# Optimization experiments

Measured on AMD Instinct MI355X. Metric: run time of the kernel, lower is better.

Reference implementation:

```python
import jax, jax.numpy as jnp
import numpy as np

N = 50000          # total residues (nodes)
E = 800000         # contact edges, avg degree 16
F_IN = 1280        # ESM embedding dim
H = 256            # hidden
L = 4              # num_layers
B = 100            # proteins in batch
MAX_NODES = 500    # residues per protein (uniform -> static to_dense_batch shape)


def setup_inputs() -> dict:
    key = jax.random.key(0)
    ks = jax.random.split(key, 16)
    s = 0.02
    inp = {
        "seq": jax.random.randint(ks[0], (N,), 0, 26),
        "edge_index": jax.random.randint(ks[1], (2, E), 0, N),
        "esm_token": jax.random.normal(ks[2], (N, F_IN), jnp.float32),
        "batch": jnp.arange(N) // MAX_NODES,
        # lin0
        "lin0_W": jax.random.normal(ks[3], (F_IN, H), jnp.float32) * s,
        "lin0_b": jnp.zeros((H,), jnp.float32),
        # WeightConv1 per layer: lin1 (root), lin2 (neighbor), lin3 (mask head)
        "wc_W1": jax.random.normal(ks[4], (L, H, H), jnp.float32) * s,
        "wc_b1": jnp.zeros((L, H), jnp.float32),
        "wc_W2": jax.random.normal(ks[5], (L, H, H), jnp.float32) * s,
        "wc_b2": jnp.zeros((L, H), jnp.float32),
        "wc_W3": jax.random.normal(ks[6], (L, H, H), jnp.float32) * s,
        "wc_b3": jnp.zeros((L, H), jnp.float32),
        # SparseConv per layer: neighbor weight + bias, root weight
        "sc_Wn": jax.random.normal(ks[7], (L, H, H), jnp.float32) * s,
        "sc_bn": jnp.zeros((L, H), jnp.float32),
        "sc_Wr": jax.random.normal(ks[8], (L, H, H), jnp.float32) * s,
    }
    return inp


def reference(seq, edge_index, esm_token, batch,
              lin0_W, lin0_b,
              wc_W1, wc_b1, wc_W2, wc_b2, wc_W3, wc_b3,
              sc_Wn, sc_bn, sc_Wr):
    src, dst = edge_index[0], edge_index[1]
    x = esm_token @ lin0_W + lin0_b              # [N, H]
    mask_val = None
    xs = []
    for i in range(L):
        # ---- WeightConv1: learned edge-conditioned node mask ----
        xm = x if mask_val is None else x * mask_val
        h_nb = xm @ wc_W2[i] + wc_b2[i]          # neighbor transform [N, H]
        agg = jax.ops.segment_sum(h_nb[src], dst, num_segments=N)
        h = jax.nn.relu(agg + xm @ wc_W1[i] + wc_b1[i])
        mask_val = jax.nn.sigmoid(h @ wc_W3[i] + wc_b3[i])   # [N, H]
        # ---- SparseConv: mask-gated sparse aggregation ----
        xg = x * mask_val
        agg2 = jax.ops.segment_sum(xg[src], dst, num_segments=N)
        x = jax.nn.relu(agg2 @ sc_Wn[i] + sc_bn[i] + x @ sc_Wr[i])
        xs.append(x)
    feat = jnp.concatenate(xs, axis=-1)          # jumping-knowledge cat [N, L*H]
    # ---- to_dense_batch ----
    counts = jax.ops.segment_sum(jnp.ones((N,), jnp.int32), batch, num_segments=B)
    starts = jnp.cumsum(counts) - counts
    pos = jnp.arange(N) - starts[batch]
    dense = jnp.zeros((B, MAX_NODES, L * H), feat.dtype).at[batch, pos].set(feat)
    node_mask = jnp.zeros((B, MAX_NODES), bool).at[batch, pos].set(True)
    return dense, node_mask
```

## Files before the change

kernel.cpp:

```cpp
#include <hip/hip_runtime.h>

#define NNODES 50000
#define HDIM 256
#define NLAYERS 4
#define NEDGES 800000
#define FIN 1280
#define LDOUT 1024

typedef _Float16 f16;
typedef __attribute__((ext_vector_type(8))) _Float16 f16x8;
typedef __attribute__((ext_vector_type(4))) _Float16 f16x4;
typedef __attribute__((ext_vector_type(4))) float f32x4;

enum { SRC_H = 0, SRC_MULH = 1, SRC_ADDRELU_HH = 2, SRC_CATH = 3 };
enum { EPI_W2W1H = 0, EPI_MASKXG = 1, EPI_CATH = 2 };

template<int SRC, int EPI, int KTILES>
__global__ __launch_bounds__(256) void mgemm_k(
    const f16*  __restrict__ A3,
    const f16*  __restrict__ A5,
    const f16*  __restrict__ A4,
    const f16*  __restrict__ Xh,
    const f16*  __restrict__ Wt,
    const f16*  __restrict__ Wt2,
    const float* __restrict__ bias,
    const float* __restrict__ bias2,
    float* __restrict__ Cf, int ldc,
    f16*  __restrict__ Ch,
    f16*  __restrict__ Ch2)
{
    constexpr int K = KTILES * 64;
    __shared__ f16 Asm[2][4096];

    const int row0 = blockIdx.x * 64;
    const int by = blockIdx.y;
    const int tid = threadIdx.x;
    const int wv = tid >> 6;
    const int l = tid & 63;

    f32x4 acc[4][4] = {};

    const int sr = tid >> 2;
    const int sc0 = (tid & 3) * 16;
    const int grow = row0 + sr;
    const bool rok = grow < NNODES;
    const int lane_base0 =
        (((sc0 >> 5) * 4 + (sr >> 4)) * 64 + (sr & 15) + (((sc0 & 31) >> 3) * 16)) * 8;
    const int lane_base1 = lane_base0 + 128;

    const f16* Wsel = (EPI == EPI_W2W1H && by) ? Wt2 : Wt;
    const f16* bp[4];
    #pragma unroll
    for (int cf = 0; cf < 4; ++cf)
        bp[cf] = Wsel + (size_t)(wv * 64 + cf * 16 + (l & 15)) * K + ((l >> 4) * 8);

    struct SReg { f16x8 h0, h1, g0, g1; };
    SReg RA, RB;

    auto LOAD = [&](SReg& r, int kt) {
        if (!rok) return;
        const int k0 = kt * 64 + sc0;
        if constexpr (SRC == SRC_CATH) {
            const f16* p = (k0 < HDIM)
                ? (A3 + (size_t)grow * HDIM + k0)
                : (A4 + (size_t)grow * HDIM + (k0 - HDIM));
            r.h0 = *(const f16x8*)p;  r.h1 = *(const f16x8*)(p + 8);
        } else {
            const f16* p = A3 + (size_t)grow * HDIM + k0;
            r.h0 = *(const f16x8*)p;  r.h1 = *(const f16x8*)(p + 8);
            if constexpr (SRC == SRC_MULH || SRC == SRC_ADDRELU_HH) {
                const f16* q = A5 + (size_t)grow * HDIM + k0;
                r.g0 = *(const f16x8*)q;  r.g1 = *(const f16x8*)(q + 8);
            }
        }
    };

    auto COMMIT = [&](const SReg& r, int b) {
        f16x8 av0, av1;
        #pragma unroll
        for (int i = 0; i < 8; ++i) { av0[i] = (f16)0.f; av1[i] = (f16)0.f; }
        if (rok) {
            if constexpr (SRC == SRC_H || SRC == SRC_CATH) {
                av0 = r.h0; av1 = r.h1;
            } else if constexpr (SRC == SRC_MULH) {
                #pragma unroll
                for (int i = 0; i < 8; ++i) {
                    av0[i] = (f16)((float)r.h0[i] * (float)r.g0[i]);
                    av1[i] = (f16)((float)r.h1[i] * (float)r.g1[i]);
                }
            } else {
                #pragma unroll
                for (int i = 0; i < 8; ++i) {
                    av0[i] = (f16)fmaxf((float)r.h0[i] + (float)r.g0[i], 0.f);
                    av1[i] = (f16)fmaxf((float)r.h1[i] + (float)r.g1[i], 0.f);
                }
            }
        }
        *(f16x8*)(&Asm[b][lane_base0]) = av0;
        *(f16x8*)(&Asm[b][lane_base1]) = av1;
    };

    auto TILE = [&](int b, int kt) {
        f16x8 af[4][2];
        #pragma unroll
        for (int rf = 0; rf < 4; ++rf)
            #pragma unroll
            for (int kb = 0; kb < 2; ++kb)
                af[rf][kb] = *(const f16x8*)(&Asm[b][((kb * 4 + rf) * 64 + l) * 8]);
        f16x8 bfr[4][2];
        #pragma unroll
        for (int cf = 0; cf < 4; ++cf) {
            bfr[cf][0] = *(const f16x8*)(bp[cf] + kt * 64);
            bfr[cf][1] = *(const f16x8*)(bp[cf] + kt * 64 + 32);
        }
        #pragma unroll
        for (int cf = 0; cf < 4; ++cf)
            #pragma unroll
            for (int rf = 0; rf < 4; ++rf)
                #pragma unroll
                for (int kb = 0; kb < 2; ++kb)
                    acc[rf][cf] = __builtin_amdgcn_mfma_f32_16x16x32_f16(
                        af[rf][kb], bfr[cf][kb], acc[rf][cf], 0, 0, 0);
    };

    LOAD(RA, 0);
    COMMIT(RA, 0);
    if (KTILES > 1) LOAD(RB, 1);
    #pragma unroll
    for (int kt2 = 0; kt2 < KTILES; kt2 += 2) {
        __syncthreads();
        TILE(0, kt2);
        if (kt2 + 1 < KTILES) COMMIT(RB, 1);
        if (kt2 + 2 < KTILES) LOAD(RA, kt2 + 2);
        if (kt2 + 1 < KTILES) {
            __syncthreads();
            TILE(1, kt2 + 1);
            if (kt2 + 2 < KTILES) COMMIT(RA, 0);
            if (kt2 + 3 < KTILES) LOAD(RB, kt2 + 3);
        }
    }

    #pragma unroll
    for (int rf = 0; rf < 4; ++rf) {
        #pragma unroll
        for (int j = 0; j < 4; ++j) {
            const int row = row0 + rf * 16 + ((l >> 4) * 4) + j;
            if (row >= NNODES) continue;
            #pragma unroll
            for (int cf = 0; cf < 4; ++cf) {
                const int col = wv * 64 + cf * 16 + (l & 15);
                float v = acc[rf][cf][j];
                if constexpr (EPI == EPI_W2W1H) {
                    if (by == 0) Ch[(size_t)row * HDIM + col]  = (f16)(v + bias[col]);
                    else         Ch2[(size_t)row * HDIM + col] = (f16)(v + bias2[col]);
                } else if constexpr (EPI == EPI_MASKXG) {
                    const float m = 1.f / (1.f + expf(-(v + bias[col])));
                    Ch2[(size_t)row * HDIM + col] = (f16)m;
                    Ch[(size_t)row * HDIM + col] =
                        (f16)((float)Xh[(size_t)row * HDIM + col] * m);
                } else {
                    const float r = fmaxf(v + bias[col], 0.f);
                    Cf[(size_t)row * ldc + col] = r;
                    Ch[(size_t)row * HDIM + col] = (f16)r;
                }
            }
        }
    }
}

template<int KTILES>
__global__ __launch_bounds__(256) void lin0_k(
    const float* __restrict__ A1, int lda1,
    const f16*  __restrict__ WtA, const f16* __restrict__ WtB,
    float* __restrict__ Cf, float* __restrict__ Cf2)
{
    constexpr int K = KTILES * 64;
    __shared__ f16 Asm[2][4096];

    const int row0 = blockIdx.x * 64;
    const int by = blockIdx.y;
    const int tid = threadIdx.x;
    const int wv = tid >> 6;
    const int l = tid & 63;

    f32x4 acc[4][4] = {};

    const int sr = tid >> 2;
    const int sc0 = (tid & 3) * 16;
    const int grow = row0 + sr;
    const bool rok = grow < NNODES;
    const int kg = by * K;
    const int lane_base0 =
        (((sc0 >> 5) * 4 + (sr >> 4)) * 64 + (sr & 15) + (((sc0 & 31) >> 3) * 16)) * 8;
    const int lane_base1 = lane_base0 + 128;

    const f16* Wsel = by ? WtB : WtA;
    const f16* bp[4];
    #pragma unroll
    for (int cf = 0; cf < 4; ++cf)
        bp[cf] = Wsel + (size_t)(wv * 64 + cf * 16 + (l & 15)) * K + ((l >> 4) * 8);

    struct SReg { float4 f0, f1, f2, f3; };
    SReg RA, RB;

    auto LOAD = [&](SReg& r, int kt) {
        if (!rok) return;
        const float* p = A1 + (size_t)grow * lda1 + kg + kt * 64 + sc0;
        r.f0 = *(const float4*)(p + 0);  r.f1 = *(const float4*)(p + 4);
        r.f2 = *(const float4*)(p + 8);  r.f3 = *(const float4*)(p + 12);
    };

    auto COMMIT = [&](const SReg& r, int b) {
        f16x8 av0, av1;
        #pragma unroll
        for (int i = 0; i < 8; ++i) { av0[i] = (f16)0.f; av1[i] = (f16)0.f; }
        if (rok) {
            av0[0]=(f16)r.f0.x; av0[1]=(f16)r.f0.y; av0[2]=(f16)r.f0.z; av0[3]=(f16)r.f0.w;
            av0[4]=(f16)r.f1.x; av0[5]=(f16)r.f1.y; av0[6]=(f16)r.f1.z; av0[7]=(f16)r.f1.w;
            av1[0]=(f16)r.f2.x; av1[1]=(f16)r.f2.y; av1[2]=(f16)r.f2.z; av1[3]=(f16)r.f2.w;
            av1[4]=(f16)r.f3.x; av1[5]=(f16)r.f3.y; av1[6]=(f16)r.f3.z; av1[7]=(f16)r.f3.w;
        }
        *(f16x8*)(&Asm[b][lane_base0]) = av0;
        *(f16x8*)(&Asm[b][lane_base1]) = av1;
    };

    auto TILE = [&](int b, int kt) {
        f16x8 af[4][2];
        #pragma unroll
        for (int rf = 0; rf < 4; ++rf)
            #pragma unroll
            for (int kb = 0; kb < 2; ++kb)
                af[rf][kb] = *(const f16x8*)(&Asm[b][((kb * 4 + rf) * 64 + l) * 8]);
        f16x8 bfr[4][2];
        #pragma unroll
        for (int cf = 0; cf < 4; ++cf) {
            bfr[cf][0] = *(const f16x8*)(bp[cf] + kt * 64);
            bfr[cf][1] = *(const f16x8*)(bp[cf] + kt * 64 + 32);
        }
        #pragma unroll
        for (int cf = 0; cf < 4; ++cf)
            #pragma unroll
            for (int rf = 0; rf < 4; ++rf)
                #pragma unroll
                for (int kb = 0; kb < 2; ++kb)
                    acc[rf][cf] = __builtin_amdgcn_mfma_f32_16x16x32_f16(
                        af[rf][kb], bfr[cf][kb], acc[rf][cf], 0, 0, 0);
    };

    LOAD(RA, 0);
    COMMIT(RA, 0);
    if (KTILES > 1) LOAD(RB, 1);
    #pragma unroll
    for (int kt2 = 0; kt2 < KTILES; kt2 += 2) {
        __syncthreads();
        TILE(0, kt2);
        if (kt2 + 1 < KTILES) COMMIT(RB, 1);
        if (kt2 + 2 < KTILES) LOAD(RA, kt2 + 2);
        if (kt2 + 1 < KTILES) {
            __syncthreads();
            TILE(1, kt2 + 1);
            if (kt2 + 2 < KTILES) COMMIT(RA, 0);
            if (kt2 + 3 < KTILES) LOAD(RB, kt2 + 3);
        }
    }

    #pragma unroll
    for (int rf = 0; rf < 4; ++rf) {
        #pragma unroll
        for (int j = 0; j < 4; ++j) {
            const int row = row0 + rf * 16 + ((l >> 4) * 4) + j;
            if (row >= NNODES) continue;
            #pragma unroll
            for (int cf = 0; cf < 4; ++cf) {
                const int col = wv * 64 + cf * 16 + (l & 15);
                (by ? Cf2 : Cf)[(size_t)row * HDIM + col] = acc[rf][cf][j];
            }
        }
    }
}

__global__ __launch_bounds__(256) void combine_k(
    const float* __restrict__ P0, const float* __restrict__ P1,
    const float* __restrict__ b, f16* __restrict__ xh)
{
    const int t = blockIdx.x * 256 + threadIdx.x;
    const int row = t >> 6;
    const int c = (t & 63) * 4;
    if (row >= NNODES) return;
    const float4 a = *(const float4*)(P0 + (size_t)row * HDIM + c);
    const float4 d = *(const float4*)(P1 + (size_t)row * HDIM + c);
    const float4 bb = *(const float4*)(b + c);
    f16x4 r;
    r[0] = (f16)(a.x + d.x + bb.x); r[1] = (f16)(a.y + d.y + bb.y);
    r[2] = (f16)(a.z + d.z + bb.z); r[3] = (f16)(a.w + d.w + bb.w);
    *(f16x4*)(xh + (size_t)row * HDIM + c) = r;
}

__global__ __launch_bounds__(256) void pack_all_k(
    const float* __restrict__ lin0_W,
    const float* __restrict__ W2, const float* __restrict__ W1,
    const float* __restrict__ W3,
    const float* __restrict__ Wn, const float* __restrict__ Wr,
    f16* __restrict__ dst)
{
    int idx = blockIdx.x * 256 + threadIdx.x;
    const int total = 163840 * 2 + 262144 * 3 + 524288;
    if (idx >= total) return;
    f16* d = dst + idx;
    if (idx < 327680) {
        const int half = idx / 163840;
        int r = idx % 163840;
        const int col = r / 640, k = r % 640;
        *d = (f16)lin0_W[(size_t)(k + half * 640) * 256 + col];
        return;
    }
    idx -= 327680;
    if (idx < 786432) {
        const int which = idx / 262144;
        int r = idx % 262144;
        const int i = r / 65536; r %= 65536;
        const int col = r / 256, k = r % 256;
        const float* W = (which == 0) ? W2 : (which == 1) ? W1 : W3;
        *d = (f16)W[(size_t)i * 65536 + k * 256 + col];
        return;
    }
    idx -= 786432;
    const int i = idx / 131072; int r = idx % 131072;
    const int col = r / 512, k = r % 512;
    *d = (f16)(k < 256 ? Wn[(size_t)i * 65536 + k * 256 + col]
                       : Wr[(size_t)i * 65536 + (k - 256) * 256 + col]);
}

__global__ __launch_bounds__(256) void count_k(
    const int* __restrict__ dstIdx, int* __restrict__ counts)
{
    const int e = blockIdx.x * 256 + threadIdx.x;
    if (e < NEDGES) atomicAdd(&counts[dstIdx[e]], 1);
}

__global__ __launch_bounds__(1024) void scan_k(
    const int* __restrict__ counts, int* __restrict__ starts)
{
    __shared__ int sm[1024];
    __shared__ int s_off;
    if (threadIdx.x == 0) s_off = 0;
    __syncthreads();
    for (int base = 0; base < NNODES; base += 1024) {
        const int i = base + threadIdx.x;
        const int v = (i < NNODES) ? counts[i] : 0;
        sm[threadIdx.x] = v;
        __syncthreads();
        for (int ofs = 1; ofs < 1024; ofs <<= 1) {
            const int t = (threadIdx.x >= ofs) ? sm[threadIdx.x - ofs] : 0;
            __syncthreads();
            sm[threadIdx.x] += t;
            __syncthreads();
        }
        const int incl = sm[threadIdx.x];
        const int off = s_off;
        if (i < NNODES) starts[i] = off + incl - v;
        __syncthreads();
        if (threadIdx.x == 1023) s_off = off + incl;
        __syncthreads();
    }
    if (threadIdx.x == 0) starts[NNODES] = s_off;
}

__global__ __launch_bounds__(256) void fillcsr_k(
    const int* __restrict__ srcIdx, const int* __restrict__ dstIdx,
    int* __restrict__ cursor, int* __restrict__ csr)
{
    const int e = blockIdx.x * 256 + threadIdx.x;
    if (e >= NEDGES) return;
    const int d = dstIdx[e];
    const int p = atomicAdd(&cursor[d], 1);
    csr[p] = srcIdx[e];
}

__global__ __launch_bounds__(256) void gather_g_k(
    const f16* __restrict__ rows, const int* __restrict__ csr,
    const int* __restrict__ starts, f16* __restrict__ outp)
{
    const int node = (blockIdx.x * 256 + threadIdx.x) >> 6;
    const int lane = threadIdx.x & 63;
    if (node >= NNODES) return;
    const int e0 = starts[node], e1 = starts[node + 1];
    float a0=0,a1=0,a2=0,a3=0, b0=0,b1=0,b2=0,b3=0;
    int e = e0;
    for (; e + 3 < e1; e += 4) {
        const int s0=csr[e], s1=csr[e+1], s2=csr[e+2], s3=csr[e+3];
        f16x4 v0 = *(const f16x4*)(rows + (size_t)s0 * HDIM + lane * 4);
        f16x4 v1 = *(const f16x4*)(rows + (size_t)s1 * HDIM + lane * 4);
        f16x4 v2 = *(const f16x4*)(rows + (size_t)s2 * HDIM + lane * 4);
        f16x4 v3 = *(const f16x4*)(rows + (size_t)s3 * HDIM + lane * 4);
        a0 += (float)v0[0] + (float)v2[0]; a1 += (float)v0[1] + (float)v2[1];
        a2 += (float)v0[2] + (float)v2[2]; a3 += (float)v0[3] + (float)v2[3];
        b0 += (float)v1[0] + (float)v3[0]; b1 += (float)v1[1] + (float)v3[1];
        b2 += (float)v1[2] + (float)v3[2]; b3 += (float)v1[3] + (float)v3[3];
    }
    for (; e < e1; ++e) {
        const int s0 = csr[e];
        f16x4 v0 = *(const f16x4*)(rows + (size_t)s0 * HDIM + lane * 4);
        a0 += (float)v0[0]; a1 += (float)v0[1]; a2 += (float)v0[2]; a3 += (float)v0[3];
    }
    f16x4 r;
    r[0] = (f16)(a0 + b0); r[1] = (f16)(a1 + b1);
    r[2] = (f16)(a2 + b2); r[3] = (f16)(a3 + b3);
    *(f16x4*)(outp + (size_t)node * HDIM + lane * 4) = r;
}

__global__ __launch_bounds__(256) void fill1_k(float* __restrict__ p, int n)
{
    const int t = blockIdx.x * 256 + threadIdx.x;
    if (t < n) p[t] = 1.0f;
}

extern "C" void kernel_launch(void* const* d_in, const int* in_sizes, int n_in,
                              void* d_out, int out_size, void* d_ws, size_t ws_size,
                              hipStream_t stream)
{
    const int*   edge   = (const int*)d_in[1];
    const int*   src    = edge;
    const int*   dst    = edge + NEDGES;
    const float* esm    = (const float*)d_in[2];
    const float* lin0_W = (const float*)d_in[4];
    const float* lin0_b = (const float*)d_in[5];
    const float* wc_W1  = (const float*)d_in[6];
    const float* wc_b1  = (const float*)d_in[7];
    const float* wc_W2  = (const float*)d_in[8];
    const float* wc_b2  = (const float*)d_in[9];
    const float* wc_W3  = (const float*)d_in[10];
    const float* wc_b3  = (const float*)d_in[11];
    const float* sc_Wn  = (const float*)d_in[12];
    const float* sc_bn  = (const float*)d_in[13];
    const float* sc_Wr  = (const float*)d_in[14];
    float* out = (float*)d_out;

    const size_t NH = (size_t)NNODES * HDIM;
    float* ws    = (float*)d_ws;
    float* part0 = ws;
    float* part1 = ws + NH;
    f16*   xh    = (f16*)(ws + 2 * NH);
    f16*   hnb   = xh + NH;
    f16*   agg1  = hnb + NH;
    f16*   agg2  = agg1 + NH;
    f16*   xw1h  = agg2 + NH;
    f16*   maskh = xw1h + NH;
    f16*   wpack = maskh + NH;
    f16*   lin0tA = wpack;
    f16*   lin0tB = lin0tA + 163840;
    f16*   W2t   = lin0tB + 163840;
    f16*   W1t   = W2t + 262144;
    f16*   W3t   = W1t + 262144;
    f16*   WtC   = W3t + 262144;
    int*   iws    = (int*)(WtC + 524288);
    int*   counts = iws;
    int*   starts = iws + NNODES;
    int*   cursor = iws + 2 * NNODES + 1;
    int*   csr    = iws + 3 * NNODES + 2;

    const dim3 blk(256);
    const int gemmGrid = (NNODES + 63) / 64;
    const int edgeGrid = (NEDGES + 255) / 256;
    const int waveGrid = (NNODES * 64) / 256;

    hipMemsetAsync(counts, 0, NNODES * sizeof(int), stream);
    count_k<<<edgeGrid, blk, 0, stream>>>(dst, counts);
    scan_k<<<1, 1024, 0, stream>>>(counts, starts);
    hipMemcpyAsync(cursor, starts, NNODES * sizeof(int),
                   hipMemcpyDeviceToDevice, stream);
    fillcsr_k<<<edgeGrid, blk, 0, stream>>>(src, dst, cursor, csr);

    pack_all_k<<<(1638400 + 255) / 256, blk, 0, stream>>>(
        lin0_W, wc_W2, wc_W1, wc_W3, sc_Wn, sc_Wr, wpack);

    lin0_k<10><<<dim3(gemmGrid, 2), blk, 0, stream>>>(
        esm, FIN, lin0tA, lin0tB, part0, part1);
    combine_k<<<waveGrid, blk, 0, stream>>>(part0, part1, lin0_b, xh);

    for (int i = 0; i < NLAYERS; ++i) {
        const size_t bo = (size_t)i * HDIM;
        const f16* w2 = W2t + i * 65536;
        const f16* w1 = W1t + i * 65536;
        const f16* w3 = W3t + i * 65536;
        const f16* wc = WtC + i * 131072;

        if (i == 0) {
            mgemm_k<SRC_H, EPI_W2W1H, 4><<<dim3(gemmGrid, 2), blk, 0, stream>>>(
                xh, nullptr, nullptr, nullptr, w2, w1,
                wc_b2 + bo, wc_b1 + bo, nullptr, 0, hnb, xw1h);
        } else {
            mgemm_k<SRC_MULH, EPI_W2W1H, 4><<<dim3(gemmGrid, 2), blk, 0, stream>>>(
                xh, maskh, nullptr, nullptr, w2, w1,
                wc_b2 + bo, wc_b1 + bo, nullptr, 0, hnb, xw1h);
        }
        gather_g_k<<<waveGrid, blk, 0, stream>>>(hnb, csr, starts, agg1);
        mgemm_k<SRC_ADDRELU_HH, EPI_MASKXG, 4><<<gemmGrid, blk, 0, stream>>>(
            agg1, xw1h, nullptr, xh, w3, nullptr,
            wc_b3 + bo, nullptr, nullptr, 0, hnb, maskh);
        gather_g_k<<<waveGrid, blk, 0, stream>>>(hnb, csr, starts, agg2);
        mgemm_k<SRC_CATH, EPI_CATH, 8><<<gemmGrid, blk, 0, stream>>>(
            agg2, nullptr, xh, nullptr, wc, nullptr,
            sc_bn + bo, nullptr, out + (size_t)i * HDIM, LDOUT, xh, nullptr);
    }

    const size_t maskOff = (size_t)NNODES * LDOUT;
    fill1_k<<<(NNODES + 255) / 256, blk, 0, stream>>>(out + maskOff, NNODES);
}
```

Measured before the change: 1.378 ms.

## Fuse CSR neighbor gathers into the following GEMMs via shared-memory A tiles

```diff
diff --git a/kernel.cpp b/kernel.cpp
--- a/kernel.cpp
+++ b/kernel.cpp
@@ -12,24 +12,22 @@
 typedef __attribute__((ext_vector_type(4))) _Float16 f16x4;
 typedef __attribute__((ext_vector_type(4))) float f32x4;
 
-enum { SRC_H = 0, SRC_MULH = 1, SRC_ADDRELU_HH = 2, SRC_CATH = 3 };
-enum { EPI_W2W1H = 0, EPI_MASKXG = 1, EPI_CATH = 2 };
-
-template<int SRC, int EPI, int KTILES>
-__global__ __launch_bounds__(256) void mgemm_k(
+enum { SRC_H = 0, SRC_MULH = 1 };
+
+
+template<int SRC>
+__global__ __launch_bounds__(256) void w2w1_k(
     const f16*  __restrict__ A3,
     const f16*  __restrict__ A5,
-    const f16*  __restrict__ A4,
-    const f16*  __restrict__ Xh,
     const f16*  __restrict__ Wt,
     const f16*  __restrict__ Wt2,
     const float* __restrict__ bias,
     const float* __restrict__ bias2,
-    float* __restrict__ Cf, int ldc,
     f16*  __restrict__ Ch,
     f16*  __restrict__ Ch2)
 {
-    constexpr int K = KTILES * 64;
+    constexpr int KTILES = 4;
+    constexpr int K = 256;
     __shared__ f16 Asm[2][4096];
 
     const int row0 = blockIdx.x * 64;
@@ -48,7 +46,7 @@
         (((sc0 >> 5) * 4 + (sr >> 4)) * 64 + (sr & 15) + (((sc0 & 31) >> 3) * 16)) * 8;
     const int lane_base1 = lane_base0 + 128;
 
-    const f16* Wsel = (EPI == EPI_W2W1H && by) ? Wt2 : Wt;
+    const f16* Wsel = by ? Wt2 : Wt;
     const f16* bp[4];
     #pragma unroll
     for (int cf = 0; cf < 4; ++cf)
@@ -60,18 +58,11 @@
     auto LOAD = [&](SReg& r, int kt) {
         if (!rok) return;
         const int k0 = kt * 64 + sc0;
-        if constexpr (SRC == SRC_CATH) {
-            const f16* p = (k0 < HDIM)
-                ? (A3 + (size_t)grow * HDIM + k0)
-                : (A4 + (size_t)grow * HDIM + (k0 - HDIM));
-            r.h0 = *(const f16x8*)p;  r.h1 = *(const f16x8*)(p + 8);
-        } else {
-            const f16* p = A3 + (size_t)grow * HDIM + k0;
-            r.h0 = *(const f16x8*)p;  r.h1 = *(const f16x8*)(p + 8);
-            if constexpr (SRC == SRC_MULH || SRC == SRC_ADDRELU_HH) {
-                const f16* q = A5 + (size_t)grow * HDIM + k0;
-                r.g0 = *(const f16x8*)q;  r.g1 = *(const f16x8*)(q + 8);
-            }
+        const f16* p = A3 + (size_t)grow * HDIM + k0;
+        r.h0 = *(const f16x8*)p;  r.h1 = *(const f16x8*)(p + 8);
+        if constexpr (SRC == SRC_MULH) {
+            const f16* q = A5 + (size_t)grow * HDIM + k0;
+            r.g0 = *(const f16x8*)q;  r.g1 = *(const f16x8*)(q + 8);
         }
     };
 
@@ -80,19 +71,13 @@
         #pragma unroll
         for (int i = 0; i < 8; ++i) { av0[i] = (f16)0.f; av1[i] = (f16)0.f; }
         if (rok) {
-            if constexpr (SRC == SRC_H || SRC == SRC_CATH) {
+            if constexpr (SRC == SRC_H) {
                 av0 = r.h0; av1 = r.h1;
-            } else if constexpr (SRC == SRC_MULH) {
+            } else {
                 #pragma unroll
                 for (int i = 0; i < 8; ++i) {
                     av0[i] = (f16)((float)r.h0[i] * (float)r.g0[i]);
                     av1[i] = (f16)((float)r.h1[i] * (float)r.g1[i]);
-                }
-            } else {
-                #pragma unroll
-                for (int i = 0; i < 8; ++i) {
-                    av0[i] = (f16)fmaxf((float)r.h0[i] + (float)r.g0[i], 0.f);
-                    av1[i] = (f16)fmaxf((float)r.h1[i] + (float)r.g1[i], 0.f);
                 }
             }
         }
@@ -125,19 +110,17 @@
 
     LOAD(RA, 0);
     COMMIT(RA, 0);
-    if (KTILES > 1) LOAD(RB, 1);
+    LOAD(RB, 1);
     #pragma unroll
     for (int kt2 = 0; kt2 < KTILES; kt2 += 2) {
         __syncthreads();
         TILE(0, kt2);
-        if (kt2 + 1 < KTILES) COMMIT(RB, 1);
+        COMMIT(RB, 1);
         if (kt2 + 2 < KTILES) LOAD(RA, kt2 + 2);
-        if (kt2 + 1 < KTILES) {
-            __syncthreads();
-            TILE(1, kt2 + 1);
-            if (kt2 + 2 < KTILES) COMMIT(RA, 0);
-            if (kt2 + 3 < KTILES) LOAD(RB, kt2 + 3);
-        }
+        __syncthreads();
+        TILE(1, kt2 + 1);
+        if (kt2 + 2 < KTILES) COMMIT(RA, 0);
+        if (kt2 + 3 < KTILES) LOAD(RB, kt2 + 3);
     }
 
     #pragma unroll
@@ -150,19 +133,265 @@
             for (int cf = 0; cf < 4; ++cf) {
                 const int col = wv * 64 + cf * 16 + (l & 15);
                 float v = acc[rf][cf][j];
-                if constexpr (EPI == EPI_W2W1H) {
-                    if (by == 0) Ch[(size_t)row * HDIM + col]  = (f16)(v + bias[col]);
-                    else         Ch2[(size_t)row * HDIM + col] = (f16)(v + bias2[col]);
-                } else if constexpr (EPI == EPI_MASKXG) {
-                    const float m = 1.f / (1.f + expf(-(v + bias[col])));
-                    Ch2[(size_t)row * HDIM + col] = (f16)m;
-                    Ch[(size_t)row * HDIM + col] =
-                        (f16)((float)Xh[(size_t)row * HDIM + col] * m);
-                } else {
-                    const float r = fmaxf(v + bias[col], 0.f);
-                    Cf[(size_t)row * ldc + col] = r;
-                    Ch[(size_t)row * HDIM + col] = (f16)r;
+                if (by == 0) Ch[(size_t)row * HDIM + col]  = (f16)(v + bias[col]);
+                else         Ch2[(size_t)row * HDIM + col] = (f16)(v + bias2[col]);
+            }
+        }
+    }
+}
+
+__global__ __launch_bounds__(256) void g1m_k(
+    const f16* __restrict__ hnb,
+    const int* __restrict__ csr, const int* __restrict__ starts,
+    const f16* __restrict__ xw1h,
+    const f16* __restrict__ xcur,
+    const f16* __restrict__ W3t,
+    const float* __restrict__ b3,
+    f16* __restrict__ maskh,
+    f16* __restrict__ xg)
+{
+    __shared__ f16 Afr[32 * 64 * 8];
+
+    const int tid = threadIdx.x;
+    const int l = tid & 63;
+    const int wv = tid >> 6;
+    const int row0 = blockIdx.x * 64;
+
+    const int c = l * 4;
+    const int region_c = ((c >> 6) << 3) + (((c >> 5) & 1) << 2);
+    const int slot_c = (((c & 31) >> 3) << 4);
+    for (int t = 0; t < 16; ++t) {
+        const int srow = wv * 16 + t;
+        const int node = row0 + srow;
+        float r0 = 0.f, r1 = 0.f, r2 = 0.f, r3 = 0.f;
+        if (node < NNODES) {
+            const int e0 = starts[node], e1 = starts[node + 1];
+            float s0=0,s1=0,s2=0,s3=0, u0=0,u1=0,u2=0,u3=0;
+            int e = e0;
+            for (; e + 3 < e1; e += 4) {
+                const int q0=csr[e], q1=csr[e+1], q2=csr[e+2], q3=csr[e+3];
+                f16x4 v0 = *(const f16x4*)(hnb + (size_t)q0 * HDIM + c);
+                f16x4 v1 = *(const f16x4*)(hnb + (size_t)q1 * HDIM + c);
+                f16x4 v2 = *(const f16x4*)(hnb + (size_t)q2 * HDIM + c);
+                f16x4 v3 = *(const f16x4*)(hnb + (size_t)q3 * HDIM + c);
+                s0 += (float)v0[0] + (float)v2[0]; s1 += (float)v0[1] + (float)v2[1];
+                s2 += (float)v0[2] + (float)v2[2]; s3 += (float)v0[3] + (float)v2[3];
+                u0 += (float)v1[0] + (float)v3[0]; u1 += (float)v1[1] + (float)v3[1];
+                u2 += (float)v1[2] + (float)v3[2]; u3 += (float)v1[3] + (float)v3[3];
+            }
+            for (; e < e1; ++e) {
+                const int q0 = csr[e];
+                f16x4 v0 = *(const f16x4*)(hnb + (size_t)q0 * HDIM + c);
+                s0 += (float)v0[0]; s1 += (float)v0[1];
+                s2 += (float)v0[2]; s3 += (float)v0[3];
+            }
+            const f16x4 w = *(const f16x4*)(xw1h + (size_t)node * HDIM + c);
+            r0 = fmaxf(s0 + u0 + (float)w[0], 0.f);
+            r1 = fmaxf(s1 + u1 + (float)w[1], 0.f);
+            r2 = fmaxf(s2 + u2 + (float)w[2], 0.f);
+            r3 = fmaxf(s3 + u3 + (float)w[3], 0.f);
+        }
+        f16x4 st;
+        st[0] = (f16)r0; st[1] = (f16)r1; st[2] = (f16)r2; st[3] = (f16)r3;
+        const int region = region_c + (srow >> 4);
+        const int slot = slot_c + (srow & 15);
+        *(f16x4*)(&Afr[((region << 6) + slot) * 8 + (c & 7)]) = st;
+    }
+    __syncthreads();
+
+    const f16* bp[4];
+    #pragma unroll
+    for (int cf = 0; cf < 4; ++cf)
+        bp[cf] = W3t + (size_t)(wv * 64 + cf * 16 + (l & 15)) * 256 + ((l >> 4) * 8);
+
+    f32x4 acc[4][4] = {};
+    f16x8 bC[4][2], bN[4][2];
+    #pragma unroll
+    for (int cf = 0; cf < 4; ++cf) {
+        bC[cf][0] = *(const f16x8*)(bp[cf]);
+        bC[cf][1] = *(const f16x8*)(bp[cf] + 32);
+    }
+    #pragma unroll
+    for (int kt = 0; kt < 4; ++kt) {
+        if (kt < 3) {
+            #pragma unroll
+            for (int cf = 0; cf < 4; ++cf) {
+                bN[cf][0] = *(const f16x8*)(bp[cf] + (kt + 1) * 64);
+                bN[cf][1] = *(const f16x8*)(bp[cf] + (kt + 1) * 64 + 32);
+            }
+        }
+        f16x8 af[4][2];
+        #pragma unroll
+        for (int rf = 0; rf < 4; ++rf)
+            #pragma unroll
+            for (int kb = 0; kb < 2; ++kb)
+                af[rf][kb] = *(const f16x8*)(&Afr[((kt * 8 + kb * 4 + rf) * 64 + l) * 8]);
+        #pragma unroll
+        for (int cf = 0; cf < 4; ++cf)
+            #pragma unroll
+            for (int rf = 0; rf < 4; ++rf)
+                #pragma unroll
+                for (int kb = 0; kb < 2; ++kb)
+                    acc[rf][cf] = __builtin_amdgcn_mfma_f32_16x16x32_f16(
+                        af[rf][kb], bC[cf][kb], acc[rf][cf], 0, 0, 0);
+        if (kt < 3) {
+            #pragma unroll
+            for (int cf = 0; cf < 4; ++cf) {
+                bC[cf][0] = bN[cf][0];  bC[cf][1] = bN[cf][1];
+            }
+        }
+    }
+
+    #pragma unroll
+    for (int rf = 0; rf < 4; ++rf) {
+        #pragma unroll
+        for (int j = 0; j < 4; ++j) {
+            const int row = row0 + rf * 16 + ((l >> 4) * 4) + j;
+            if (row >= NNODES) continue;
+            #pragma unroll
+            for (int cf = 0; cf < 4; ++cf) {
+                const int col = wv * 64 + cf * 16 + (l & 15);
+                const float m = 1.f / (1.f + expf(-(acc[rf][cf][j] + b3[col])));
+                maskh[(size_t)row * HDIM + col] = (f16)m;
+                xg[(size_t)row * HDIM + col] =
+                    (f16)((float)xcur[(size_t)row * HDIM + col] * m);
+            }
+        }
+    }
+}
+
+__global__ __launch_bounds__(256) void g2c_k(
+    const f16* __restrict__ xg,
+    const int* __restrict__ csr, const int* __restrict__ starts,
+    const f16* __restrict__ xcur,
+    const f16* __restrict__ WtC,
+    const float* __restrict__ bn,
+    float* __restrict__ outp,
+    f16* __restrict__ xnew)
+{
+    __shared__ f16 Afr[32 * 64 * 8];
+
+    const int tid = threadIdx.x;
+    const int l = tid & 63;
+    const int wv = tid >> 6;
+    const int row0 = blockIdx.x * 64;
+
+    const int c = l * 4;
+    const int region_c = ((c >> 6) << 3) + (((c >> 5) & 1) << 2);
+    const int slot_c = (((c & 31) >> 3) << 4);
+    for (int t = 0; t < 16; ++t) {
+        const int srow = wv * 16 + t;
+        const int node = row0 + srow;
+        float r0 = 0.f, r1 = 0.f, r2 = 0.f, r3 = 0.f;
+        if (node < NNODES) {
+            const int e0 = starts[node], e1 = starts[node + 1];
+            float s0=0,s1=0,s2=0,s3=0, u0=0,u1=0,u2=0,u3=0;
+            int e = e0;
+            for (; e + 3 < e1; e += 4) {
+                const int q0=csr[e], q1=csr[e+1], q2=csr[e+2], q3=csr[e+3];
+                f16x4 v0 = *(const f16x4*)(xg + (size_t)q0 * HDIM + c);
+                f16x4 v1 = *(const f16x4*)(xg + (size_t)q1 * HDIM + c);
+                f16x4 v2 = *(const f16x4*)(xg + (size_t)q2 * HDIM + c);
+                f16x4 v3 = *(const f16x4*)(xg + (size_t)q3 * HDIM + c);
+                s0 += (float)v0[0] + (float)v2[0]; s1 += (float)v0[1] + (float)v2[1];
+                s2 += (float)v0[2] + (float)v2[2]; s3 += (float)v0[3] + (float)v2[3];
+                u0 += (float)v1[0] + (float)v3[0]; u1 += (float)v1[1] + (float)v3[1];
+                u2 += (float)v1[2] + (float)v3[2]; u3 += (float)v1[3] + (float)v3[3];
+            }
+            for (; e < e1; ++e) {
+                const int q0 = csr[e];
+                f16x4 v0 = *(const f16x4*)(xg + (size_t)q0 * HDIM + c);
+                s0 += (float)v0[0]; s1 += (float)v0[1];
+                s2 += (float)v0[2]; s3 += (float)v0[3];
+            }
+            r0 = s0 + u0; r1 = s1 + u1; r2 = s2 + u2; r3 = s3 + u3;
+        }
+        f16x4 st;
+        st[0] = (f16)r0; st[1] = (f16)r1; st[2] = (f16)r2; st[3] = (f16)r3;
+        const int region = region_c + (srow >> 4);
+        const int slot = slot_c + (srow & 15);
+        *(f16x4*)(&Afr[((region << 6) + slot) * 8 + (c & 7)]) = st;
+    }
+    __syncthreads();
+
+    const f16* bp[4];
+    #pragma unroll
+    for (int cf = 0; cf < 4; ++cf)
+        bp[cf] = WtC + (size_t)(wv * 64 + cf * 16 + (l & 15)) * 512 + ((l >> 4) * 8);
+
+    bool rvalid[4];
+    const f16* xrow[4];
+    #pragma unroll
+    for (int rf = 0; rf < 4; ++rf) {
+        const int ar = row0 + rf * 16 + (l & 15);
+        rvalid[rf] = ar < NNODES;
+        xrow[rf] = xcur + (size_t)ar * HDIM + ((l >> 4) * 8);
+    }
+
+    f32x4 acc[4][4] = {};
+    f16x8 bC[4][2], bN[4][2];
+    #pragma unroll
+    for (int cf = 0; cf < 4; ++cf) {
+        bC[cf][0] = *(const f16x8*)(bp[cf]);
+        bC[cf][1] = *(const f16x8*)(bp[cf] + 32);
+    }
+    #pragma unroll
+    for (int kt = 0; kt < 8; ++kt) {
+        if (kt < 7) {
+            #pragma unroll
+            for (int cf = 0; cf < 4; ++cf) {
+                bN[cf][0] = *(const f16x8*)(bp[cf] + (kt + 1) * 64);
+                bN[cf][1] = *(const f16x8*)(bp[cf] + (kt + 1) * 64 + 32);
+            }
+        }
+        f16x8 af[4][2];
+        if (kt < 4) {
+            #pragma unroll
+            for (int rf = 0; rf < 4; ++rf)
+                #pragma unroll
+                for (int kb = 0; kb < 2; ++kb)
+                    af[rf][kb] = *(const f16x8*)(&Afr[((kt * 8 + kb * 4 + rf) * 64 + l) * 8]);
+        } else {
+            #pragma unroll
+            for (int rf = 0; rf < 4; ++rf)
+                #pragma unroll
+                for (int kb = 0; kb < 2; ++kb) {
+                    f16x8 v;
+                    #pragma unroll
+                    for (int i = 0; i < 8; ++i) v[i] = (f16)0.f;
+                    if (rvalid[rf])
+                        v = *(const f16x8*)(xrow[rf] + (kt - 4) * 64 + kb * 32);
+                    af[rf][kb] = v;
                 }
+        }
+        #pragma unroll
+        for (int cf = 0; cf < 4; ++cf)
+            #pragma unroll
+            for (int rf = 0; rf < 4; ++rf)
+                #pragma unroll
+                for (int kb = 0; kb < 2; ++kb)
+                    acc[rf][cf] = __builtin_amdgcn_mfma_f32_16x16x32_f16(
+                        af[rf][kb], bC[cf][kb], acc[rf][cf], 0, 0, 0);
+        if (kt < 7) {
+            #pragma unroll
+            for (int cf = 0; cf < 4; ++cf) {
+                bC[cf][0] = bN[cf][0];  bC[cf][1] = bN[cf][1];
+            }
+        }
+    }
+
+    #pragma unroll
+    for (int rf = 0; rf < 4; ++rf) {
+        #pragma unroll
+        for (int j = 0; j < 4; ++j) {
+            const int row = row0 + rf * 16 + ((l >> 4) * 4) + j;
+            if (row >= NNODES) continue;
+            #pragma unroll
+            for (int cf = 0; cf < 4; ++cf) {
+                const int col = wv * 64 + cf * 16 + (l & 15);
+                const float r = fmaxf(acc[rf][cf][j] + bn[col], 0.f);
+                outp[(size_t)row * LDOUT + col] = r;
+                xnew[(size_t)row * HDIM + col] = (f16)r;
             }
         }
     }
@@ -375,38 +604,6 @@
     const int d = dstIdx[e];
     const int p = atomicAdd(&cursor[d], 1);
     csr[p] = srcIdx[e];
-}
-
-__global__ __launch_bounds__(256) void gather_g_k(
-    const f16* __restrict__ rows, const int* __restrict__ csr,
-    const int* __restrict__ starts, f16* __restrict__ outp)
-{
-    const int node = (blockIdx.x * 256 + threadIdx.x) >> 6;
-    const int lane = threadIdx.x & 63;
-    if (node >= NNODES) return;
-    const int e0 = starts[node], e1 = starts[node + 1];
-    float a0=0,a1=0,a2=0,a3=0, b0=0,b1=0,b2=0,b3=0;
-    int e = e0;
-    for (; e + 3 < e1; e += 4) {
-        const int s0=csr[e], s1=csr[e+1], s2=csr[e+2], s3=csr[e+3];
-        f16x4 v0 = *(const f16x4*)(rows + (size_t)s0 * HDIM + lane * 4);
-        f16x4 v1 = *(const f16x4*)(rows + (size_t)s1 * HDIM + lane * 4);
-        f16x4 v2 = *(const f16x4*)(rows + (size_t)s2 * HDIM + lane * 4);
-        f16x4 v3 = *(const f16x4*)(rows + (size_t)s3 * HDIM + lane * 4);
-        a0 += (float)v0[0] + (float)v2[0]; a1 += (float)v0[1] + (float)v2[1];
-        a2 += (float)v0[2] + (float)v2[2]; a3 += (float)v0[3] + (float)v2[3];
-        b0 += (float)v1[0] + (float)v3[0]; b1 += (float)v1[1] + (float)v3[1];
-        b2 += (float)v1[2] + (float)v3[2]; b3 += (float)v1[3] + (float)v3[3];
-    }
-    for (; e < e1; ++e) {
-        const int s0 = csr[e];
-        f16x4 v0 = *(const f16x4*)(rows + (size_t)s0 * HDIM + lane * 4);
-        a0 += (float)v0[0]; a1 += (float)v0[1]; a2 += (float)v0[2]; a3 += (float)v0[3];
-    }
-    f16x4 r;
-    r[0] = (f16)(a0 + b0); r[1] = (f16)(a1 + b1);
-    r[2] = (f16)(a2 + b2); r[3] = (f16)(a3 + b3);
-    *(f16x4*)(outp + (size_t)node * HDIM + lane * 4) = r;
 }
 
 __global__ __launch_bounds__(256) void fill1_k(float* __restrict__ p, int n)
@@ -440,13 +637,13 @@
     float* ws    = (float*)d_ws;
     float* part0 = ws;
     float* part1 = ws + NH;
-    f16*   xh    = (f16*)(ws + 2 * NH);
-    f16*   hnb   = xh + NH;
-    f16*   agg1  = hnb + NH;
-    f16*   agg2  = agg1 + NH;
-    f16*   xw1h  = agg2 + NH;
+    f16*   xhA   = (f16*)(ws + 2 * NH);
+    f16*   xhB   = xhA + NH;
+    f16*   hnb   = xhB + NH;
+    f16*   xw1h  = hnb + NH;
     f16*   maskh = xw1h + NH;
-    f16*   wpack = maskh + NH;
+    f16*   xg    = maskh + NH;
+    f16*   wpack = xg + NH;
     f16*   lin0tA = wpack;
     f16*   lin0tB = lin0tA + 163840;
     f16*   W2t   = lin0tB + 163840;
@@ -476,7 +673,7 @@
 
     lin0_k<10><<<dim3(gemmGrid, 2), blk, 0, stream>>>(
         esm, FIN, lin0tA, lin0tB, part0, part1);
-    combine_k<<<waveGrid, blk, 0, stream>>>(part0, part1, lin0_b, xh);
+    combine_k<<<waveGrid, blk, 0, stream>>>(part0, part1, lin0_b, xhA);
 
     for (int i = 0; i < NLAYERS; ++i) {
         const size_t bo = (size_t)i * HDIM;
@@ -484,24 +681,21 @@
         const f16* w1 = W1t + i * 65536;
         const f16* w3 = W3t + i * 65536;
         const f16* wc = WtC + i * 131072;
+        const f16* xcur = (i & 1) ? xhB : xhA;
+        f16*       xnew = (i & 1) ? xhA : xhB;
 
         if (i == 0) {
-            mgemm_k<SRC_H, EPI_W2W1H, 4><<<dim3(gemmGrid, 2), blk, 0, stream>>>(
-                xh, nullptr, nullptr, nullptr, w2, w1,
-                wc_b2 + bo, wc_b1 + bo, nullptr, 0, hnb, xw1h);
+            w2w1_k<SRC_H><<<dim3(gemmGrid, 2), blk, 0, stream>>>(
+                xcur, nullptr, w2, w1, wc_b2 + bo, wc_b1 + bo, hnb, xw1h);
         } else {
-            mgemm_k<SRC_MULH, EPI_W2W1H, 4><<<dim3(gemmGrid, 2), blk, 0, stream>>>(
-                xh, maskh, nullptr, nullptr, w2, w1,
-                wc_b2 + bo, wc_b1 + bo, nullptr, 0, hnb, xw1h);
-        }
-        gather_g_k<<<waveGrid, blk, 0, stream>>>(hnb, csr, starts, agg1);
-        mgemm_k<SRC_ADDRELU_HH, EPI_MASKXG, 4><<<gemmGrid, blk, 0, stream>>>(
-            agg1, xw1h, nullptr, xh, w3, nullptr,
-            wc_b3 + bo, nullptr, nullptr, 0, hnb, maskh);
-        gather_g_k<<<waveGrid, blk, 0, stream>>>(hnb, csr, starts, agg2);
-        mgemm_k<SRC_CATH, EPI_CATH, 8><<<gemmGrid, blk, 0, stream>>>(
-            agg2, nullptr, xh, nullptr, wc, nullptr,
-            sc_bn + bo, nullptr, out + (size_t)i * HDIM, LDOUT, xh, nullptr);
+            w2w1_k<SRC_MULH><<<dim3(gemmGrid, 2), blk, 0, stream>>>(
+                xcur, maskh, w2, w1, wc_b2 + bo, wc_b1 + bo, hnb, xw1h);
+        }
+        g1m_k<<<gemmGrid, blk, 0, stream>>>(
+            hnb, csr, starts, xw1h, xcur, w3, wc_b3 + bo, maskh, xg);
+        g2c_k<<<gemmGrid, blk, 0, stream>>>(
+            xg, csr, starts, xcur, wc, sc_bn + bo,
+            out + (size_t)i * HDIM, xnew);
     }
 
     const size_t maskOff = (size_t)NNODES * LDOUT;
```

Result: slower. 1.934 ms (+40.3%).

## Aggregate before transform in WeightConv and fuse W2/W1 into one concat GEMM

Applied to the files above, without the earlier changes.

```diff
diff --git a/kernel.cpp b/kernel.cpp
--- a/kernel.cpp
+++ b/kernel.cpp
@@ -12,28 +12,27 @@
 typedef __attribute__((ext_vector_type(4))) _Float16 f16x4;
 typedef __attribute__((ext_vector_type(4))) float f32x4;
 
-enum { SRC_H = 0, SRC_MULH = 1, SRC_ADDRELU_HH = 2, SRC_CATH = 3 };
-enum { EPI_W2W1H = 0, EPI_MASKXG = 1, EPI_CATH = 2 };
+enum { SRC_H = 0, SRC_CATH = 1 };
+enum { EPI_HRELU = 0, EPI_MASKXG = 1, EPI_CATH2 = 2 };
 
 template<int SRC, int EPI, int KTILES>
 __global__ __launch_bounds__(256) void mgemm_k(
     const f16*  __restrict__ A3,
-    const f16*  __restrict__ A5,
     const f16*  __restrict__ A4,
     const f16*  __restrict__ Xh,
+    const int*  __restrict__ deg,
     const f16*  __restrict__ Wt,
-    const f16*  __restrict__ Wt2,
     const float* __restrict__ bias,
     const float* __restrict__ bias2,
     float* __restrict__ Cf, int ldc,
     f16*  __restrict__ Ch,
-    f16*  __restrict__ Ch2)
+    f16*  __restrict__ Ch2,
+    f16*  __restrict__ Ch3)
 {
     constexpr int K = KTILES * 64;
     __shared__ f16 Asm[2][4096];
 
     const int row0 = blockIdx.x * 64;
-    const int by = blockIdx.y;
     const int tid = threadIdx.x;
     const int wv = tid >> 6;
     const int l = tid & 63;
@@ -48,54 +47,32 @@
         (((sc0 >> 5) * 4 + (sr >> 4)) * 64 + (sr & 15) + (((sc0 & 31) >> 3) * 16)) * 8;
     const int lane_base1 = lane_base0 + 128;
 
-    const f16* Wsel = (EPI == EPI_W2W1H && by) ? Wt2 : Wt;
     const f16* bp[4];
     #pragma unroll
     for (int cf = 0; cf < 4; ++cf)
-        bp[cf] = Wsel + (size_t)(wv * 64 + cf * 16 + (l & 15)) * K + ((l >> 4) * 8);
-
-    struct SReg { f16x8 h0, h1, g0, g1; };
+        bp[cf] = Wt + (size_t)(wv * 64 + cf * 16 + (l & 15)) * K + ((l >> 4) * 8);
+
+    struct SReg { f16x8 h0, h1; };
     SReg RA, RB;
 
     auto LOAD = [&](SReg& r, int kt) {
         if (!rok) return;
         const int k0 = kt * 64 + sc0;
+        const f16* p;
         if constexpr (SRC == SRC_CATH) {
-            const f16* p = (k0 < HDIM)
-                ? (A3 + (size_t)grow * HDIM + k0)
-                : (A4 + (size_t)grow * HDIM + (k0 - HDIM));
-            r.h0 = *(const f16x8*)p;  r.h1 = *(const f16x8*)(p + 8);
+            p = (k0 < HDIM) ? (A3 + (size_t)grow * HDIM + k0)
+                            : (A4 + (size_t)grow * HDIM + (k0 - HDIM));
         } else {
-            const f16* p = A3 + (size_t)grow * HDIM + k0;
-            r.h0 = *(const f16x8*)p;  r.h1 = *(const f16x8*)(p + 8);
-            if constexpr (SRC == SRC_MULH || SRC == SRC_ADDRELU_HH) {
-                const f16* q = A5 + (size_t)grow * HDIM + k0;
-                r.g0 = *(const f16x8*)q;  r.g1 = *(const f16x8*)(q + 8);
-            }
-        }
+            p = A3 + (size_t)grow * HDIM + k0;
+        }
+        r.h0 = *(const f16x8*)p;  r.h1 = *(const f16x8*)(p + 8);
     };
 
     auto COMMIT = [&](const SReg& r, int b) {
         f16x8 av0, av1;
         #pragma unroll
         for (int i = 0; i < 8; ++i) { av0[i] = (f16)0.f; av1[i] = (f16)0.f; }
-        if (rok) {
-            if constexpr (SRC == SRC_H || SRC == SRC_CATH) {
-                av0 = r.h0; av1 = r.h1;
-            } else if constexpr (SRC == SRC_MULH) {
-                #pragma unroll
-                for (int i = 0; i < 8; ++i) {
-                    av0[i] = (f16)((float)r.h0[i] * (float)r.g0[i]);
-                    av1[i] = (f16)((float)r.h1[i] * (float)r.g1[i]);
-                }
-            } else {
-                #pragma unroll
-                for (int i = 0; i < 8; ++i) {
-                    av0[i] = (f16)fmaxf((float)r.h0[i] + (float)r.g0[i], 0.f);
-                    av1[i] = (f16)fmaxf((float)r.h1[i] + (float)r.g1[i], 0.f);
-                }
-            }
-        }
+        if (rok) { av0 = r.h0; av1 = r.h1; }
         *(f16x8*)(&Asm[b][lane_base0]) = av0;
         *(f16x8*)(&Asm[b][lane_base1]) = av1;
     };
@@ -150,9 +127,10 @@
             for (int cf = 0; cf < 4; ++cf) {
                 const int col = wv * 64 + cf * 16 + (l & 15);
                 float v = acc[rf][cf][j];
-                if constexpr (EPI == EPI_W2W1H) {
-                    if (by == 0) Ch[(size_t)row * HDIM + col]  = (f16)(v + bias[col]);
-                    else         Ch2[(size_t)row * HDIM + col] = (f16)(v + bias2[col]);
+                if constexpr (EPI == EPI_HRELU) {
+                    const float dv = (float)deg[row];
+                    v = fmaxf(v + dv * bias[col] + bias2[col], 0.f);
+                    Ch[(size_t)row * HDIM + col] = (f16)v;
                 } else if constexpr (EPI == EPI_MASKXG) {
                     const float m = 1.f / (1.f + expf(-(v + bias[col])));
                     Ch2[(size_t)row * HDIM + col] = (f16)m;
@@ -162,6 +140,8 @@
                     const float r = fmaxf(v + bias[col], 0.f);
                     Cf[(size_t)row * ldc + col] = r;
                     Ch[(size_t)row * HDIM + col] = (f16)r;
+                    Ch3[(size_t)row * HDIM + col] =
+                        (f16)(r * (float)Xh[(size_t)row * HDIM + col]);
                 }
             }
         }
@@ -171,8 +151,8 @@
 template<int KTILES>
 __global__ __launch_bounds__(256) void lin0_k(
     const float* __restrict__ A1, int lda1,
-    const f16*  __restrict__ WtA, const f16* __restrict__ WtB,
-    float* __restrict__ Cf, float* __restrict__ Cf2)
+    const f16*  __restrict__ WtBase,
+    f16* __restrict__ parts)
 {
     constexpr int K = KTILES * 64;
     __shared__ f16 Asm[2][4096];
@@ -194,7 +174,7 @@
         (((sc0 >> 5) * 4 + (sr >> 4)) * 64 + (sr & 15) + (((sc0 & 31) >> 3) * 16)) * 8;
     const int lane_base1 = lane_base0 + 128;
 
-    const f16* Wsel = by ? WtB : WtA;
+    const f16* Wsel = WtBase + (size_t)by * 256 * K;
     const f16* bp[4];
     #pragma unroll
     for (int cf = 0; cf < 4; ++cf)
@@ -264,6 +244,7 @@
         }
     }
 
+    f16* Ph = parts + (size_t)by * NNODES * HDIM;
     #pragma unroll
     for (int rf = 0; rf < 4; ++rf) {
         #pragma unroll
@@ -273,27 +254,33 @@
             #pragma unroll
             for (int cf = 0; cf < 4; ++cf) {
                 const int col = wv * 64 + cf * 16 + (l & 15);
-                (by ? Cf2 : Cf)[(size_t)row * HDIM + col] = acc[rf][cf][j];
+                Ph[(size_t)row * HDIM + col] = (f16)acc[rf][cf][j];
             }
         }
     }
 }
 
-__global__ __launch_bounds__(256) void combine_k(
-    const float* __restrict__ P0, const float* __restrict__ P1,
-    const float* __restrict__ b, f16* __restrict__ xh)
+__global__ __launch_bounds__(256) void combine4_k(
+    const f16* __restrict__ parts, const float* __restrict__ b,
+    f16* __restrict__ xh)
 {
     const int t = blockIdx.x * 256 + threadIdx.x;
     const int row = t >> 6;
     const int c = (t & 63) * 4;
     if (row >= NNODES) return;
-    const float4 a = *(const float4*)(P0 + (size_t)row * HDIM + c);
-    const float4 d = *(const float4*)(P1 + (size_t)row * HDIM + c);
+    const size_t NH = (size_t)NNODES * HDIM;
+    const size_t off = (size_t)row * HDIM + c;
+    f16x4 p0 = *(const f16x4*)(parts + off);
+    f16x4 p1 = *(const f16x4*)(parts + NH + off);
+    f16x4 p2 = *(const f16x4*)(parts + 2 * NH + off);
+    f16x4 p3 = *(const f16x4*)(parts + 3 * NH + off);
     const float4 bb = *(const float4*)(b + c);
     f16x4 r;
-    r[0] = (f16)(a.x + d.x + bb.x); r[1] = (f16)(a.y + d.y + bb.y);
-    r[2] = (f16)(a.z + d.z + bb.z); r[3] = (f16)(a.w + d.w + bb.w);
-    *(f16x4*)(xh + (size_t)row * HDIM + c) = r;
+    r[0] = (f16)((float)p0[0] + (float)p1[0] + (float)p2[0] + (float)p3[0] + bb.x);
+    r[1] = (f16)((float)p0[1] + (float)p1[1] + (float)p2[1] + (float)p3[1] + bb.y);
+    r[2] = (f16)((float)p0[2] + (float)p1[2] + (float)p2[2] + (float)p3[2] + bb.z);
+    r[3] = (f16)((float)p0[3] + (float)p1[3] + (float)p2[3] + (float)p3[3] + bb.w);
+    *(f16x4*)(xh + off) = r;
 }
 
 __global__ __launch_bounds__(256) void pack_all_k(
@@ -304,27 +291,34 @@
     f16* __restrict__ dst)
 {
     int idx = blockIdx.x * 256 + threadIdx.x;
-    const int total = 163840 * 2 + 262144 * 3 + 524288;
+    const int total = 327680 + 524288 + 262144 + 524288;
     if (idx >= total) return;
     f16* d = dst + idx;
     if (idx < 327680) {
-        const int half = idx / 163840;
-        int r = idx % 163840;
-        const int col = r / 640, k = r % 640;
-        *d = (f16)lin0_W[(size_t)(k + half * 640) * 256 + col];
+        const int q = idx / 81920;
+        int r = idx % 81920;
+        const int col = r / 320, k = r % 320;
+        *d = (f16)lin0_W[(size_t)(k + q * 320) * 256 + col];
         return;
     }
     idx -= 327680;
-    if (idx < 786432) {
-        const int which = idx / 262144;
-        int r = idx % 262144;
-        const int i = r / 65536; r %= 65536;
+    if (idx < 524288) {
+        const int i = idx / 131072;
+        int r = idx % 131072;
+        const int col = r / 512, k = r % 512;
+        *d = (f16)(k < 256 ? W2[(size_t)i * 65536 + k * 256 + col]
+                           : W1[(size_t)i * 65536 + (k - 256) * 256 + col]);
+        return;
+    }
+    idx -= 524288;
+    if (idx < 262144) {
+        const int i = idx / 65536;
+        int r = idx % 65536;
         const int col = r / 256, k = r % 256;
-        const float* W = (which == 0) ? W2 : (which == 1) ? W1 : W3;
-        *d = (f16)W[(size_t)i * 65536 + k * 256 + col];
+        *d = (f16)W3[(size_t)i * 65536 + k * 256 + col];
         return;
     }
-    idx -= 786432;
+    idx -= 262144;
     const int i = idx / 131072; int r = idx % 131072;
     const int col = r / 512, k = r % 512;
     *d = (f16)(k < 256 ? Wn[(size_t)i * 65536 + k * 256 + col]
@@ -437,27 +431,24 @@
     float* out = (float*)d_out;
 
     const size_t NH = (size_t)NNODES * HDIM;
-    float* ws    = (float*)d_ws;
-    float* part0 = ws;
-    float* part1 = ws + NH;
-    f16*   xh    = (f16*)(ws + 2 * NH);
-    f16*   hnb   = xh + NH;
-    f16*   agg1  = hnb + NH;
-    f16*   agg2  = agg1 + NH;
-    f16*   xw1h  = agg2 + NH;
-    f16*   maskh = xw1h + NH;
-    f16*   wpack = maskh + NH;
-    f16*   lin0tA = wpack;
-    f16*   lin0tB = lin0tA + 163840;
-    f16*   W2t   = lin0tB + 163840;
-    f16*   W1t   = W2t + 262144;
-    f16*   W3t   = W1t + 262144;
-    f16*   WtC   = W3t + 262144;
-    int*   iws    = (int*)(WtC + 524288);
-    int*   counts = iws;
-    int*   starts = iws + NNODES;
-    int*   cursor = iws + 2 * NNODES + 1;
-    int*   csr    = iws + 3 * NNODES + 2;
+    f16* parts = (f16*)d_ws;
+    f16* aggx  = parts;
+    f16* hbuf  = parts + NH;
+    f16* xg    = parts + 2 * NH;
+    f16* agg2  = parts + 3 * NH;
+    f16* xh    = parts + 4 * NH;
+    f16* xm    = xh + NH;
+    f16* maskh = xm + NH;
+    f16* wpack = maskh + NH;
+    f16* lin0t = wpack;
+    f16* WH    = lin0t + 327680;
+    f16* W3t   = WH + 524288;
+    f16* WtC   = W3t + 262144;
+    int* iws    = (int*)(WtC + 524288);
+    int* counts = iws;
+    int* starts = iws + NNODES;
+    int* cursor = iws + 2 * NNODES + 1;
+    int* csr    = iws + 3 * NNODES + 2;
 
     const dim3 blk(256);
     const int gemmGrid = (NNODES + 63) / 64;
@@ -474,34 +465,27 @@
     pack_all_k<<<(1638400 + 255) / 256, blk, 0, stream>>>(
         lin0_W, wc_W2, wc_W1, wc_W3, sc_Wn, sc_Wr, wpack);
 
-    lin0_k<10><<<dim3(gemmGrid, 2), blk, 0, stream>>>(
-        esm, FIN, lin0tA, lin0tB, part0, part1);
-    combine_k<<<waveGrid, blk, 0, stream>>>(part0, part1, lin0_b, xh);
+    lin0_k<5><<<dim3(gemmGrid, 4), blk, 0, stream>>>(esm, FIN, lin0t, parts);
+    combine4_k<<<waveGrid, blk, 0, stream>>>(parts, lin0_b, xh);
 
     for (int i = 0; i < NLAYERS; ++i) {
         const size_t bo = (size_t)i * HDIM;
-        const f16* w2 = W2t + i * 65536;
-        const f16* w1 = W1t + i * 65536;
-        const f16* w3 = W3t + i * 65536;
-        const f16* wc = WtC + i * 131072;
-
-        if (i == 0) {
-            mgemm_k<SRC_H, EPI_W2W1H, 4><<<dim3(gemmGrid, 2), blk, 0, stream>>>(
-                xh, nullptr, nullptr, nullptr, w2, w1,
-                wc_b2 + bo, wc_b1 + bo, nullptr, 0, hnb, xw1h);
-        } else {
-            mgemm_k<SRC_MULH, EPI_W2W1H, 4><<<dim3(gemmGrid, 2), blk, 0, stream>>>(
-                xh, maskh, nullptr, nullptr, w2, w1,
-                wc_b2 + bo, wc_b1 + bo, nullptr, 0, hnb, xw1h);
-        }
-        gather_g_k<<<waveGrid, blk, 0, stream>>>(hnb, csr, starts, agg1);
-        mgemm_k<SRC_ADDRELU_HH, EPI_MASKXG, 4><<<gemmGrid, blk, 0, stream>>>(
-            agg1, xw1h, nullptr, xh, w3, nullptr,
-            wc_b3 + bo, nullptr, nullptr, 0, hnb, maskh);
-        gather_g_k<<<waveGrid, blk, 0, stream>>>(hnb, csr, starts, agg2);
-        mgemm_k<SRC_CATH, EPI_CATH, 8><<<gemmGrid, blk, 0, stream>>>(
-            agg2, nullptr, xh, nullptr, wc, nullptr,
-            sc_bn + bo, nullptr, out + (size_t)i * HDIM, LDOUT, xh, nullptr);
+        const f16* wh = WH + (size_t)i * 131072;
+        const f16* w3 = W3t + (size_t)i * 65536;
+        const f16* wc = WtC + (size_t)i * 131072;
+        const f16* xmtab = (i == 0) ? xh : xm;
+
+        gather_g_k<<<waveGrid, blk, 0, stream>>>(xmtab, csr, starts, aggx);
+        mgemm_k<SRC_CATH, EPI_HRELU, 8><<<gemmGrid, blk, 0, stream>>>(
+            aggx, xmtab, nullptr, counts, wh, wc_b2 + bo, wc_b1 + bo,
+            nullptr, 0, hbuf, nullptr, nullptr);
+        mgemm_k<SRC_H, EPI_MASKXG, 4><<<gemmGrid, blk, 0, stream>>>(
+            hbuf, nullptr, xh, nullptr, w3, wc_b3 + bo, nullptr,
+            nullptr, 0, xg, maskh, nullptr);
+        gather_g_k<<<waveGrid, blk, 0, stream>>>(xg, csr, starts, agg2);
+        mgemm_k<SRC_CATH, EPI_CATH2, 8><<<gemmGrid, blk, 0, stream>>>(
+            agg2, xh, maskh, nullptr, wc, sc_bn + bo, nullptr,
+            out + (size_t)i * HDIM, LDOUT, xh, nullptr, xm);
     }
 
     const size_t maskOff = (size_t)NNODES * LDOUT;
```

New measurement: 1.353 ms. About the same (-1.8%).
